# Optimization experiments

Hardware: AMD Instinct MI355X
Metric: run time of the kernel (lower is better)

Reference implementation:

```python
import jax, jax.numpy as jnp
import numpy as np

KS = 5          # kernel_size
D = 2           # spatial dim
DX = 0.01       # region kernel spacing
SCALE = 1.0
NX, NY = 32, 32
N = NX * NY


def _region_kernel():
    # gaussians.region_kernel: KS x KS grid of offsets spaced DX, centered at 0
    off = (jnp.arange(KS, dtype=jnp.float32) - (KS - 1) / 2.0) * DX
    gx, gy = jnp.meshgrid(off, off, indexing='ij')
    return jnp.stack([gx, gy], -1).reshape(-1, D)  # (KS*KS, 2)


def _build_cov(scaling, transform):
    # Cholesky-style parameterization: L lower-triangular with diag=scaling,
    # off-diag=transform; cov = L @ L^T (d=2 closed form)
    s0, s1 = scaling[:, 0], scaling[:, 1]
    t = transform[:, 0]
    c00 = s0 * s0
    c01 = s0 * t
    c11 = t * t + s1 * s1
    return jnp.stack([jnp.stack([c00, c01], -1), jnp.stack([c01, c11], -1)], -2)


def _inv2x2(c):
    det = c[:, 0, 0] * c[:, 1, 1] - c[:, 0, 1] * c[:, 1, 0]
    inv = jnp.stack([jnp.stack([c[:, 1, 1], -c[:, 0, 1]], -1),
                     jnp.stack([-c[:, 1, 0], c[:, 0, 0]], -1)], -2)
    return inv / det[:, None, None]


def setup_inputs() -> dict:
    key = jax.random.key(0)
    ks = jax.random.split(key, 20)
    # Gaussian state: grid means as in __init__
    tx = jnp.linspace(-1.0, 1.0, NX) * SCALE
    ty = jnp.linspace(-1.0, 1.0, NY) * SCALE
    gx, gy = jnp.meshgrid(tx, ty, indexing='ij')
    means = jnp.stack([gx, gy], -1).reshape(-1, D).astype(jnp.float32)
    u = 0.1 * jax.random.normal(ks[0], (N, 1), jnp.float32)
    scaling = jnp.exp(-4.5 + 0.2 * jax.random.normal(ks[1], (N, D), jnp.float32)) * SCALE
    transform = 0.002 * jax.random.normal(ks[2], (N, 1), jnp.float32)
    opacities = 2.0 + 0.1 * jax.random.normal(ks[3], (N,), jnp.float32)
    # network weights (4 heads share the first 3 layer shapes)
    convW = 0.05 * jax.random.normal(ks[4], (4, 50, 3, KS, KS), jnp.float32)
    convb = 0.01 * jax.random.normal(ks[5], (4, 50), jnp.float32)
    embW = 0.3 * jax.random.normal(ks[6], (4, 7, 30), jnp.float32)
    embb = 0.01 * jax.random.normal(ks[7], (4, 30), jnp.float32)
    l1W = 0.1 * jax.random.normal(ks[8], (4, 80, 80), jnp.float32)
    l1b = 0.01 * jax.random.normal(ks[9], (4, 80), jnp.float32)
    outW_sol = 0.1 * jax.random.normal(ks[10], (80, 1), jnp.float32)
    outb_sol = 0.01 * jax.random.normal(ks[11], (1,), jnp.float32)
    outW_trans = 0.1 * jax.random.normal(ks[12], (80, 2), jnp.float32)
    outb_trans = 0.01 * jax.random.normal(ks[13], (2,), jnp.float32)
    outW_scale = 0.1 * jax.random.normal(ks[14], (80, 2), jnp.float32)
    outb_scale = 0.01 * jax.random.normal(ks[15], (2,), jnp.float32)
    outW_tform = 0.1 * jax.random.normal(ks[16], (80, 1), jnp.float32)
    outb_tform = 0.01 * jax.random.normal(ks[17], (1,), jnp.float32)
    return {"means": means, "u": u, "scaling": scaling, "transform": transform,
            "opacities": opacities, "convW": convW, "convb": convb,
            "embW": embW, "embb": embb, "l1W": l1W, "l1b": l1b,
            "outW_sol": outW_sol, "outb_sol": outb_sol,
            "outW_trans": outW_trans, "outb_trans": outb_trans,
            "outW_scale": outW_scale, "outb_scale": outb_scale,
            "outW_tform": outW_tform, "outb_tform": outb_tform}


def reference(means, u, scaling, transform, opacities, convW, convb, embW, embb,
              l1W, l1b, outW_sol, outb_sol, outW_trans, outb_trans,
              outW_scale, outb_scale, outW_tform, outb_tform):
    n = means.shape[0]
    cov = _build_cov(scaling, transform)          # (N,2,2)
    conics = _inv2x2(cov)                         # (N,2,2)

    # --- sampling (torch.no_grad block in original) ---
    kern = _region_kernel()                                        # (25,2)
    samples = (means[:, None, :] + kern[None]).reshape(-1, D)      # (M,2), M=N*25
    bc = jnp.all(jnp.abs(samples) < SCALE, -1).astype(means.dtype)[:, None]
    alpha = jax.nn.sigmoid(opacities)                              # (N,)
    diff = samples[:, None, :] - means[None, :, :]                 # (M,N,2)
    Cq = jnp.einsum('nij,mnj->mni', conics, diff)                  # (M,N,2)
    G = jnp.exp(-0.5 * jnp.einsum('mni,mni->mn', diff, Cq)) * alpha[None, :]  # (M,N)
    u_s = G @ u                                                    # (M,1)
    # DIFFUSION pde_rhs = trace of laplacian: sum_n G * (|C q|^2 - tr(C)) * u_n
    trC = conics[:, 0, 0] + conics[:, 1, 1]
    lap = jnp.einsum('mn,mn,nc->mc', G, (Cq ** 2).sum(-1) - trC[None, :], u)  # (M,1)
    in_samples = jax.lax.stop_gradient(jnp.concatenate([u_s, lap, bc], -1))   # (M,3)

    # (N, 25, 3) -> (N, 3, 5, 5)
    img = in_samples.reshape(n, KS * KS, -1).transpose(0, 2, 1).reshape(n, -1, KS, KS)
    in_params = jnp.concatenate([means, u, scaling, transform, opacities[:, None]], -1)  # (N,7)

    # 4 Networks: conv(5x5 -> 1x1, 50ch) + param embed(7->30) + MLP(80->80->out)
    y = jnp.tanh(jnp.einsum('ncij,kocij->kno', img, convW) + convb[:, None, :])   # (4,N,50)
    e = jnp.tanh(jnp.einsum('nf,kfg->kng', in_params, embW) + embb[:, None, :])   # (4,N,30)
    h = jnp.tanh(jnp.einsum('knf,kfg->kng', jnp.concatenate([y, e], -1), l1W)
                 + l1b[:, None, :])                                               # (4,N,80)

    deltas = h[0] @ outW_sol + outb_sol          # (N,1)
    translation = h[1] @ outW_trans + outb_trans # (N,2)
    dscale = h[2] @ outW_scale + outb_scale      # (N,2)
    dtransform = h[3] @ outW_tform + outb_tform  # (N,1)

    u_new = u + deltas
    means_new = means + translation
    scaling_new = scaling * jnp.exp(dscale)
    transform_new = transform + dtransform
    cov_new = _build_cov(scaling_new, transform_new)
    return (u_new, means_new, scaling_new, transform_new, cov_new)
```

## Files before the change

### kernel.cpp

```cpp
#include <hip/hip_runtime.h>
#include <hip/hip_bf16.h>


#define NG 1024
#define GPB 2

__device__ __forceinline__ float tanh_fast(float x) {
    return 1.0f - 2.0f / (__expf(2.0f * x) + 1.0f);
}

__global__ __launch_bounds__(256, 2) void k_fused(
    const float* __restrict__ means, const float* __restrict__ u,
    const float* __restrict__ scal, const float* __restrict__ trans,
    const float* __restrict__ opac,
    const float* __restrict__ convW, const float* __restrict__ convb,
    const float* __restrict__ embW,  const float* __restrict__ embb,
    const float* __restrict__ l1W,   const float* __restrict__ l1b,
    const float* __restrict__ oWs,  const float* __restrict__ obs,
    const float* __restrict__ oWt,  const float* __restrict__ obt,
    const float* __restrict__ oWsc, const float* __restrict__ obsc,
    const float* __restrict__ oWtf, const float* __restrict__ obtf,
    float* __restrict__ out)
{
    __shared__ __align__(16) float gcomp[NG * 8];
    __shared__ float pus[2][2][32];
    __shared__ float plap[2][2][32];
    __shared__ float2 simgv[80];
    __shared__ float2 hinv[4][80];
    __shared__ float2 hvv[4 * 81];
    __shared__ float semb[840];
    __shared__ float sembb[120];
    __shared__ float shead[480];
    __shared__ float sheadb[6];
    __shared__ int   cnt;

    const int t  = threadIdx.x;
    const int n0 = blockIdx.x * GPB;

    float2 gm[4], gs[4];
    float  gt[4], go[4], gu[4];
    #pragma unroll
    for (int i = 0; i < 4; ++i) {
        int g = t + 256 * i;
        gm[i] = *(const float2*)(means + 2 * g);
        gs[i] = *(const float2*)(scal  + 2 * g);
        gt[i] = trans[g];
        go[i] = opac[g];
        gu[i] = u[g];
    }

    float se0 = embW[t];
    float se1 = embW[256 + t];
    float se2 = embW[512 + t];
    float se3 = (t < 72)  ? embW[768 + t] : 0.0f;
    float sbb = (t < 120) ? embb[t] : 0.0f;
    float sh0 = (t < 80)  ? oWs[t] : (t < 240) ? oWt[t - 80] : oWsc[t - 240];
    float sh1 = 0.0f;
    if (t < 224) sh1 = (t < 144) ? oWsc[t + 16] : oWtf[t - 144];
    float shb = 0.0f;
    if (t < 6) shb = (t == 0) ? obs[0] : (t < 3) ? obt[t-1]
                   : (t < 5) ? obsc[t-3] : obtf[0];

    const float mx0 = means[2*n0],   my0 = means[2*n0+1];
    const float mx1 = means[2*n0+2], my1 = means[2*n0+3];
    const float uu0 = u[n0],     uu1 = u[n0+1];
    const float sc00 = scal[2*n0],   sc01 = scal[2*n0+1];
    const float sc10 = scal[2*n0+2], sc11 = scal[2*n0+3];
    const float tr0 = trans[n0], tr1 = trans[n0+1];
    const float op0 = opac[n0],  op1 = opac[n0+1];

    float wcv[75];
    {
        const float* w = convW + (size_t)(t < 200 ? t : 0) * 75;
        #pragma unroll
        for (int j = 0; j < 75; ++j) wcv[j] = w[j];
    }
    float w1[80];
    {
        int k = t / 80, g = t - (t / 80) * 80;
        const float* w = l1W + (size_t)(k * 80) * 80 + g;
        #pragma unroll
        for (int f = 0; f < 80; ++f) w1[f] = w[f * 80];
    }
    float bcv  = (t < 200) ? convb[t] : 0.0f;
    float b1   = l1b[t];
    float b1k3 = l1b[256 + (t & 63)];

    const float bxmin = fminf(mx0, mx1) - 0.02f, bxmax = fmaxf(mx0, mx1) + 0.02f;
    const float bymin = fminf(my0, my1) - 0.02f, bymax = fmaxf(my0, my1) + 0.02f;

    semb[t]       = se0;
    semb[256 + t] = se1;
    semb[512 + t] = se2;
    if (t < 72)  semb[768 + t] = se3;
    if (t < 120) sembb[t] = sbb;
    shead[t] = sh0;
    if (t < 224) shead[256 + t] = sh1;
    if (t < 6)   sheadb[t] = shb;

    if (t == 0) cnt = 0;
    __syncthreads();

    #pragma unroll
    for (int i = 0; i < 4; ++i) {
        float gmx = gm[i].x, gmy = gm[i].y;
        float s0  = gs[i].x, s1  = gs[i].y;
        float tt  = gt[i];
        float c00 = s0*s0, c01 = s0*tt, c11 = tt*tt + s1*s1;
        float r2  = 100.0f * (c00 + c11);
        float ddx = fmaxf(fmaxf(bxmin - gmx, gmx - bxmax), 0.0f);
        float ddy = fmaxf(fmaxf(bymin - gmy, gmy - bymax), 0.0f);
        if (ddx*ddx + ddy*ddy <= r2) {
            float idet = 1.0f / (c00*c11 - c01*c01);
            float A = c11*idet, B = -c01*idet, C = c00*idet;
            float alpha = 1.0f / (1.0f + __expf(-go[i]));
            int slot = atomicAdd(&cnt, 1);
            float4* dst = (float4*)(gcomp + slot*8);
            dst[0] = make_float4(gmx, gmy, A, B);
            dst[1] = make_float4(C, A + C, alpha * gu[i], 0.0f);
        }
    }
    __syncthreads();
    const int nsurv = cnt;

    {
        int w = t >> 6, lane = t & 63;
        int l = w >> 1;
        int hc = ((w & 1) << 1) | (lane >> 5);
        int s  = lane & 31; if (s > 24) s = 24;
        int si = s / 5, sj = s - si * 5;
        float gx = l ? mx1 : mx0, gy = l ? my1 : my0;
        float sx = gx + (float)(si - 2) * 0.01f;
        float sy = gy + (float)(sj - 2) * 0.01f;
        float us = 0.0f, lp = 0.0f;
        #pragma unroll 2
        for (int i = hc; i < nsurv; i += 4) {
            float4 a = *(const float4*)(gcomp + i*8);
            float4 b = *(const float4*)(gcomp + i*8 + 4);
            float dx = sx - a.x, dy = sy - a.y;
            float Cq0 = a.z*dx + a.w*dy;
            float Cq1 = a.w*dx + b.x*dy;
            float q   = dx*Cq0 + dy*Cq1;
            float e   = __expf(-0.5f*q) * b.z;
            us += e;
            lp += e * (Cq0*Cq0 + Cq1*Cq1 - b.y);
        }
        us += __shfl_down(us, 32);
        lp += __shfl_down(lp, 32);
        if ((lane & 31) == s && lane < 32) {
            pus[l][w & 1][s] = us; plap[l][w & 1][s] = lp;
        }
    }
    __syncthreads();

    if (t < 50) {
        int l = t / 25, s = t - l * 25;
        float us = pus[l][0][s] + pus[l][1][s];
        float lp = plap[l][0][s] + plap[l][1][s];
        int si = s / 5, sj = s - si * 5;
        float gx = l ? mx1 : mx0, gy = l ? my1 : my0;
        float sx = gx + (float)(si - 2) * 0.01f;
        float sy = gy + (float)(sj - 2) * 0.01f;
        float* sg = (float*)simgv;
        sg[(s)*2 + l]      = us;
        sg[(25 + s)*2 + l] = lp;
        sg[(50 + s)*2 + l] = (fabsf(sx) < 1.0f && fabsf(sy) < 1.0f) ? 1.0f : 0.0f;
    }
    __syncthreads();

    if (t < 200) {
        float a0 = bcv, a1 = bcv;
        #pragma unroll
        for (int j = 0; j < 75; ++j) {
            float2 v = simgv[j];
            a0 += v.x * wcv[j];
            a1 += v.y * wcv[j];
        }
        int k = t / 50, o = t - k * 50;
        hinv[k][o] = make_float2(tanh_fast(a0), tanh_fast(a1));
    } else {
        for (int idx = t - 200; idx < 240; idx += 56) {
            int l = idx / 120, rem = idx - l * 120;
            int k = rem / 30, g = rem - k * 30;
            float acc = sembb[k * 30 + g];
            #pragma unroll
            for (int f = 0; f < 7; ++f) {
                float in0, in1;
                switch (f) {
                    case 0: in0 = mx0;  in1 = mx1;  break;
                    case 1: in0 = my0;  in1 = my1;  break;
                    case 2: in0 = uu0;  in1 = uu1;  break;
                    case 3: in0 = sc00; in1 = sc10; break;
                    case 4: in0 = sc01; in1 = sc11; break;
                    case 5: in0 = tr0;  in1 = tr1;  break;
                    default: in0 = op0; in1 = op1;  break;
                }
                acc += (l ? in1 : in0) * semb[(k*7 + f)*30 + g];
            }
            ((float*)hinv)[(k*80 + 50 + g)*2 + l] = tanh_fast(acc);
        }
    }
    __syncthreads();

    {
        int k = t / 80, g = t - (t / 80) * 80;
        float a0 = b1, a1 = b1;
        #pragma unroll
        for (int f = 0; f < 80; ++f) {
            float2 h = hinv[k][f];
            a0 += h.x * w1[f];
            a1 += h.y * w1[f];
        }
        hvv[k*81 + g] = make_float2(tanh_fast(a0), tanh_fast(a1));
    }
    if (t < 64) {
        int g = 16 + t;
        float a0 = b1k3, a1 = b1k3;
        #pragma unroll 8
        for (int f = 0; f < 80; ++f) {
            float w = l1W[(3*80 + f)*80 + g];
            float2 h = hinv[3][f];
            a0 += h.x * w;
            a1 += h.y * w;
        }
        hvv[3*81 + g] = make_float2(tanh_fast(a0), tanh_fast(a1));
    }
    __syncthreads();

    if (t < 64) {
        int l = (t / 6) & 1, t6 = t % 6;
        int k, base, stride, j;
        if (t6 == 0)      { k = 0; base = 0;   stride = 1; j = 0; }
        else if (t6 < 3)  { k = 1; base = 80;  stride = 2; j = t6 - 1; }
        else if (t6 < 5)  { k = 2; base = 240; stride = 2; j = t6 - 3; }
        else              { k = 3; base = 400; stride = 1; j = 0; }
        float acc = sheadb[t6];
        const float* hvf = (const float*)hvv;
        #pragma unroll 8
        for (int f = 0; f < 80; ++f)
            acc += hvf[(k*81 + f)*2 + l] * shead[base + f * stride + j];

        int sb = (t / 6) * 6;
        float o0 = __shfl(acc, sb + 0);
        float o1 = __shfl(acc, sb + 1);
        float o2 = __shfl(acc, sb + 2);
        float o3 = __shfl(acc, sb + 3);
        float o4 = __shfl(acc, sb + 4);
        float o5 = __shfl(acc, sb + 5);

        if (t == 0 || t == 6) {
            int n = n0 + (t / 6);
            float uu = t ? uu1 : uu0;
            float s0 = t ? sc10 : sc00, s1 = t ? sc11 : sc01;
            float tr = t ? tr1 : tr0;
            float u_new = uu + o0;
            float mxn = (t ? mx1 : mx0) + o1;
            float myn = (t ? my1 : my0) + o2;
            float s0n = s0 * __expf(o3);
            float s1n = s1 * __expf(o4);
            float tn  = tr + o5;
            float c00 = s0n*s0n, c01 = s0n*tn, c11 = tn*tn + s1n*s1n;
            out[n]              = u_new;
            out[1024 + 2*n]     = mxn;
            out[1024 + 2*n + 1] = myn;
            out[3072 + 2*n]     = s0n;
            out[3072 + 2*n + 1] = s1n;
            out[5120 + n]       = tn;
            out[6144 + 4*n]     = c00;
            out[6144 + 4*n + 1] = c01;
            out[6144 + 4*n + 2] = c01;
            out[6144 + 4*n + 3] = c11;
        }
    }
}

extern "C" void kernel_launch(void* const* d_in, const int* in_sizes, int n_in,
                              void* d_out, int out_size, void* d_ws, size_t ws_size,
                              hipStream_t stream)
{
    k_fused<<<dim3(NG / GPB), dim3(256), 0, stream>>>(
        (const float*)d_in[0],  (const float*)d_in[1],  (const float*)d_in[2],
        (const float*)d_in[3],  (const float*)d_in[4],  (const float*)d_in[5],
        (const float*)d_in[6],  (const float*)d_in[7],  (const float*)d_in[8],
        (const float*)d_in[9],  (const float*)d_in[10], (const float*)d_in[11],
        (const float*)d_in[12], (const float*)d_in[13], (const float*)d_in[14],
        (const float*)d_in[15], (const float*)d_in[16], (const float*)d_in[17],
        (const float*)d_in[18], (float*)d_out);
}
```

Measured before the change: 101.5 us.

## Split conv dot products across 4 lanes with shuffle reduction

The conv layer is re-partitioned so each group of 4 threads computes one of the 200 output channels. Each lane handles a strided quarter of the 75 inputs, and the partial sums are combined with xor shuffles. All 256 threads now take part instead of 200, and per-thread conv weight registers drop from 75 to 38, which may lower register pressure and raise occupancy. The embedding computation is also moved from the leftover 56 threads to threads 0-239 in a single pass. In exchange, some conv weights are loaded from global memory in the middle of the compute phase, and shuffle overhead is added.

```diff
diff --git a/kernel.cpp b/kernel.cpp
--- a/kernel.cpp
+++ b/kernel.cpp
@@ -36,6 +36,7 @@
 
     const int t  = threadIdx.x;
     const int n0 = blockIdx.x * GPB;
+    const int gid = t >> 2, li = t & 3;
 
     float2 gm[4], gs[4];
     float  gt[4], go[4], gu[4];
@@ -69,22 +70,31 @@
     const float tr0 = trans[n0], tr1 = trans[n0+1];
     const float op0 = opac[n0],  op1 = opac[n0+1];
 
-    float wcv[75];
-    {
-        const float* w = convW + (size_t)(t < 200 ? t : 0) * 75;
-        #pragma unroll
-        for (int j = 0; j < 75; ++j) wcv[j] = w[j];
-    }
-    float w1[80];
+    float wl1[80];
     {
         int k = t / 80, g = t - (t / 80) * 80;
         const float* w = l1W + (size_t)(k * 80) * 80 + g;
         #pragma unroll
-        for (int f = 0; f < 80; ++f) w1[f] = w[f * 80];
-    }
-    float bcv  = (t < 200) ? convb[t] : 0.0f;
+        for (int f = 0; f < 80; ++f) wl1[f] = w[f * 80];
+    }
     float b1   = l1b[t];
     float b1k3 = l1b[256 + (t & 63)];
+
+    float wa[19], wb[19];
+    {
+        const float* r0 = convW + gid * 75 + li;
+        #pragma unroll
+        for (int i = 0; i < 18; ++i) wa[i] = r0[4*i];
+        wa[18] = (li < 3) ? r0[72] : 0.0f;
+        const float* r1 = convW + (gid + 64) * 75 + li;
+        #pragma unroll
+        for (int i = 0; i < 18; ++i) wb[i] = r1[4*i];
+        wb[18] = (li < 3) ? r1[72] : 0.0f;
+    }
+    float cb0 = convb[gid];
+    float cb1 = convb[gid + 64];
+    float cb2 = convb[gid + 128];
+    float cb3 = (gid < 8) ? convb[gid + 192] : 0.0f;
 
     const float bxmin = fminf(mx0, mx1) - 0.02f, bxmax = fmaxf(mx0, mx1) + 0.02f;
     const float bymin = fminf(my0, my1) - 0.02f, bymax = fmaxf(my0, my1) + 0.02f;
@@ -168,37 +178,68 @@
     }
     __syncthreads();
 
-    if (t < 200) {
-        float a0 = bcv, a1 = bcv;
-        #pragma unroll
-        for (int j = 0; j < 75; ++j) {
-            float2 v = simgv[j];
-            a0 += v.x * wcv[j];
-            a1 += v.y * wcv[j];
-        }
-        int k = t / 50, o = t - k * 50;
-        hinv[k][o] = make_float2(tanh_fast(a0), tanh_fast(a1));
-    } else {
-        for (int idx = t - 200; idx < 240; idx += 56) {
-            int l = idx / 120, rem = idx - l * 120;
-            int k = rem / 30, g = rem - k * 30;
-            float acc = sembb[k * 30 + g];
+#define CONV_ROUND(BUF, FF, CB)                                           \
+    {                                                                     \
+        float a0 = 0.0f, a1 = 0.0f;                                       \
+        _Pragma("unroll")                                                 \
+        for (int i = 0; i < 19; ++i) {                                    \
+            a0 += sv[i].x * BUF[i];                                       \
+            a1 += sv[i].y * BUF[i];                                       \
+        }                                                                 \
+        a0 += __shfl_xor(a0, 1); a0 += __shfl_xor(a0, 2);                 \
+        a1 += __shfl_xor(a1, 1); a1 += __shfl_xor(a1, 2);                 \
+        if (li == 0) {                                                    \
+            int ff = (FF);                                                \
+            hinv[ff / 50][ff % 50] =                                      \
+                make_float2(tanh_fast(a0 + (CB)), tanh_fast(a1 + (CB))); \
+        }                                                                 \
+    }
+    {
+        float2 sv[19];
+        #pragma unroll
+        for (int i = 0; i < 19; ++i) {
+            int j = li + 4 * i;
+            sv[i] = simgv[j > 74 ? 74 : j];
+        }
+        CONV_ROUND(wa, gid, cb0)
+        {
+            const float* r2 = convW + (gid + 128) * 75 + li;
             #pragma unroll
-            for (int f = 0; f < 7; ++f) {
-                float in0, in1;
-                switch (f) {
-                    case 0: in0 = mx0;  in1 = mx1;  break;
-                    case 1: in0 = my0;  in1 = my1;  break;
-                    case 2: in0 = uu0;  in1 = uu1;  break;
-                    case 3: in0 = sc00; in1 = sc10; break;
-                    case 4: in0 = sc01; in1 = sc11; break;
-                    case 5: in0 = tr0;  in1 = tr1;  break;
-                    default: in0 = op0; in1 = op1;  break;
-                }
-                acc += (l ? in1 : in0) * semb[(k*7 + f)*30 + g];
+            for (int i = 0; i < 18; ++i) wa[i] = r2[4*i];
+            wa[18] = (li < 3) ? r2[72] : 0.0f;
+        }
+        CONV_ROUND(wb, gid + 64, cb1)
+        if (gid < 8) {
+            const float* r3 = convW + (gid + 192) * 75 + li;
+            #pragma unroll
+            for (int i = 0; i < 18; ++i) wb[i] = r3[4*i];
+            wb[18] = (li < 3) ? r3[72] : 0.0f;
+        }
+        CONV_ROUND(wa, gid + 128, cb2)
+        if (gid < 8) {
+            CONV_ROUND(wb, gid + 192, cb3)
+        }
+    }
+#undef CONV_ROUND
+    if (t < 240) {
+        int l = t / 120, rem = t - l * 120;
+        int k = rem / 30, g = rem - k * 30;
+        float acc = sembb[k * 30 + g];
+        #pragma unroll
+        for (int f = 0; f < 7; ++f) {
+            float in0, in1;
+            switch (f) {
+                case 0: in0 = mx0;  in1 = mx1;  break;
+                case 1: in0 = my0;  in1 = my1;  break;
+                case 2: in0 = uu0;  in1 = uu1;  break;
+                case 3: in0 = sc00; in1 = sc10; break;
+                case 4: in0 = sc01; in1 = sc11; break;
+                case 5: in0 = tr0;  in1 = tr1;  break;
+                default: in0 = op0; in1 = op1;  break;
             }
-            ((float*)hinv)[(k*80 + 50 + g)*2 + l] = tanh_fast(acc);
-        }
+            acc += (l ? in1 : in0) * semb[(k*7 + f)*30 + g];
+        }
+        ((float*)hinv)[(k*80 + 50 + g)*2 + l] = tanh_fast(acc);
     }
     __syncthreads();
 
@@ -208,8 +249,8 @@
         #pragma unroll
         for (int f = 0; f < 80; ++f) {
             float2 h = hinv[k][f];
-            a0 += h.x * w1[f];
-            a1 += h.y * w1[f];
+            a0 += h.x * wl1[f];
+            a1 += h.y * wl1[f];
         }
         hvv[k*81 + g] = make_float2(tanh_fast(a0), tanh_fast(a1));
     }
```

New measurement: 101.9 us. No clear change (+0.5%).
